# Kernel tuning notes

Measured on AMD Instinct MI355X. Metric: run time of the kernel, lower is better.

Reference implementation:

```python
import jax, jax.numpy as jnp
import numpy as np
from jax import lax

# db6 filters (pywt convention). rec_lo are the standard Daubechies-12 scaling coefs.
REC_LO = np.array([0.11154074335008017, 0.4946238903983854, 0.7511339080215775,
                   0.3152503517092432, -0.22626469396516913, -0.12976686756709563,
                   0.09750160558707936, 0.02752286553001629, -0.031582039318031156,
                   0.0005538422009938016, 0.004777257511010651, -0.00107730108499558])
L = 12
# qmf: rec_hi[n] = (-1)^n * rec_lo[L-1-n]
REC_HI = np.array([(-1.0)**n * REC_LO[L - 1 - n] for n in range(L)])
DEC_LO = REC_LO[::-1].copy()
DEC_HI = REC_HI[::-1].copy()
J = 8  # level1
DN = ('NCH', 'OIH', 'NCH')

def _afb(x):
    # one analysis level, symmetric padding (matches pytorch_wavelets afb1d).
    B, C, N = x.shape
    outsize = (N + L - 1) // 2
    p = 2 * (outsize - 1) - N + L
    xp = jnp.pad(x, ((0, 0), (0, 0), (p // 2, p - p // 2)), mode='symmetric')
    # torch conv1d correlates with reversed dec filters == rec filters
    k = jnp.stack([jnp.asarray(REC_LO, x.dtype), jnp.asarray(REC_HI, x.dtype)])[:, None, :]
    y = lax.conv_general_dilated(xp.reshape(B * C, 1, -1), k, (2,), 'VALID',
                                 dimension_numbers=DN)  # (B*C, 2, outsize)
    y = y.reshape(B, C, 2, outsize)
    return y[:, :, 0], y[:, :, 1]

def _sfb(lo, hi):
    # one synthesis level: conv_transpose1d(stride=2, padding=L-2) with rec filters
    # == dilate-by-2, pad 1 each side, correlate with flipped rec (= dec) filters.
    B, C, N = lo.shape
    def up(z, k):
        kk = jnp.asarray(k, z.dtype)[None, None, :]
        return lax.conv_general_dilated(z.reshape(B * C, 1, N), kk, (1,), [(1, 1)],
                                        lhs_dilation=(2,), dimension_numbers=DN).reshape(B, C, -1)
    return up(lo, DEC_LO) + up(hi, DEC_HI)  # length 2N - L + 2

def setup_inputs() -> dict:
    key = jax.random.key(0)
    k1, k2, k3 = jax.random.split(key, 3)
    Cin, Cout = 64, 64
    scale = 1.0 / (Cin * Cout)
    x = jax.random.normal(k1, (256, Cin, 1024), dtype=jnp.float32)
    weights1 = scale * jax.random.uniform(k2, (Cin, Cout, J + 6), dtype=jnp.float32)
    weights2 = scale * jax.random.uniform(k3, (Cin, Cout, J + 6), dtype=jnp.float32)
    return {'x': x, 'weights1': weights1, 'weights2': weights2}

def reference(x, weights1, weights2):
    # DWT decompose: yh[0] finest ... yh[-1] coarsest (pytorch_wavelets order)
    lo = x
    highs = []
    for _ in range(J):
        lo, hi = _afb(lo)
        highs.append(hi)
    # channel mix on coarsest approx and coarsest detail
    lo = jnp.einsum('bix,iox->box', lo, weights1)
    highs[-1] = jnp.einsum('bix,iox->box', highs[-1], weights2)
    # IDWT reconstruct, trimming odd-length mismatches like pytorch_wavelets
    y = lo
    for hi in highs[::-1]:
        if y.shape[-1] > hi.shape[-1]:
            y = y[..., :hi.shape[-1]]
        y = _sfb(y, hi)
    return y
```

## Files before the change

### kernel.cpp

```cpp
#include <hip/hip_runtime.h>

typedef float f2 __attribute__((ext_vector_type(2)));
typedef _Float16 half_t;
typedef _Float16 h4 __attribute__((ext_vector_type(4)));
typedef _Float16 h8 __attribute__((ext_vector_type(8)));

static constexpr float REC_LO[12] = {
  0.11154074335008017f, 0.4946238903983854f, 0.7511339080215775f, 0.3152503517092432f,
  -0.22626469396516913f, -0.12976686756709563f, 0.09750160558707936f, 0.02752286553001629f,
  -0.031582039318031156f, 0.0005538422009938016f, 0.004777257511010651f, -0.00107730108499558f };
static constexpr float REC_HI[12] = {
  -0.00107730108499558f, -0.004777257511010651f, 0.0005538422009938016f, 0.031582039318031156f,
  0.02752286553001629f, -0.09750160558707936f, -0.12976686756709563f, 0.22626469396516913f,
  0.3152503517092432f, -0.7511339080215775f, 0.4946238903983854f, -0.11154074335008017f };
static constexpr float DEC_LO[12] = {
  -0.00107730108499558f, 0.004777257511010651f, 0.0005538422009938016f, -0.031582039318031156f,
  0.02752286553001629f, 0.09750160558707936f, -0.12976686756709563f, -0.22626469396516913f,
  0.3152503517092432f, 0.7511339080215775f, 0.4946238903983854f, 0.11154074335008017f };
static constexpr float DEC_HI[12] = {
  -0.11154074335008017f, 0.4946238903983854f, -0.7511339080215775f, 0.3152503517092432f,
  0.22626469396516913f, -0.12976686756709563f, -0.09750160558707936f, 0.02752286553001629f,
  0.031582039318031156f, 0.0005538422009938016f, -0.004777257511010651f, -0.00107730108499558f };

#define NROWS 16384
#define WPB 4


__global__ __launch_bounds__(256) void afb_fused(const float* __restrict__ x,
                                                 half_t* __restrict__ ws) {
  __shared__ float sA[WPB][548];
  __shared__ float sB[WPB][296];
  constexpr int LENS[9] = {1024, 517, 264, 137, 74, 42, 26, 18, 14};
  constexpr int HSTR[8] = {520, 264, 144, 80, 48, 32, 24, 16};
  constexpr int HOFF[8] = {0, 520, 784, 928, 1008, 1056, 1088, 1112};
  const int wid = threadIdx.x >> 6;
  const int lane = threadIdx.x & 63;
  const int row = blockIdx.x * WPB + wid;
  float* bufA = sA[wid];
  float* bufB = sB[wid];
  const float* xrow = x + (size_t)row * 1024;
  half_t* hi0 = ws + (size_t)row * 520;

  {
    const int q = lane;
    const int base = (q == 0) ? 0 : 16 * q - 12;
    float xv[28];
#pragma unroll
    for (int r = 0; r < 7; ++r) {
      float4 v = *reinterpret_cast<const float4*>(xrow + base + 4 * r);
      xv[4 * r] = v.x; xv[4 * r + 1] = v.y; xv[4 * r + 2] = v.z; xv[4 * r + 3] = v.w;
    }
    float w[26];
    if (q == 0) {
#pragma unroll
      for (int e = 0; e < 26; ++e) w[e] = xv[e < 10 ? 9 - e : e - 10];
    } else {
#pragma unroll
      for (int e = 0; e < 26; ++e) w[e] = xv[2 + e];
    }
    f2 a[8];
#pragma unroll
    for (int d = 0; d < 8; ++d) a[d] = (f2){0.f, 0.f};
#pragma unroll
    for (int k = 0; k < 12; ++k) {
      f2 c = (f2){REC_LO[k], REC_HI[k]};
#pragma unroll
      for (int d = 0; d < 8; ++d) a[d] += w[2 * d + k] * c;
    }
#pragma unroll
    for (int d = 0; d < 4; ++d)
      *reinterpret_cast<f2*>(bufA + 14 + 8 * q + 2 * d) = (f2){a[2 * d].x, a[2 * d + 1].x};
    h8 hh;
#pragma unroll
    for (int d = 0; d < 8; ++d) hh[d] = (half_t)a[d].y;
    *reinterpret_cast<h8*>(hi0 + 8 * q) = hh;
  }
  if (lane < 5) {
    const int i0 = 1014 + 2 * lane;
    float acL = 0.f, acH = 0.f;
#pragma unroll
    for (int k = 0; k < 12; ++k) {
      int idx = i0 + k;
      idx = min(idx, 2047 - idx);
      float v = xrow[idx];
      acL += v * REC_LO[k];
      acH += v * REC_HI[k];
    }
    bufA[14 + 512 + lane] = acL;
    hi0[512 + lane] = (half_t)acH;
  }
  if (lane < 21) {
    int d, s;
    if (lane < 10) { d = 13 - lane; s = 14 + lane; }
    else { int k = lane - 10; d = 14 + 517 + k; s = 14 + 516 - k; }
    bufA[d] = bufA[s];
  }

  if (lane < 33) {
    const float* pp = bufA + 16 * lane + 4;
    float xv[28];
#pragma unroll
    for (int r = 0; r < 7; ++r) {
      float4 v = *reinterpret_cast<const float4*>(pp + 4 * r);
      xv[4 * r] = v.x; xv[4 * r + 1] = v.y; xv[4 * r + 2] = v.z; xv[4 * r + 3] = v.w;
    }
    f2 a[8];
#pragma unroll
    for (int d = 0; d < 8; ++d) a[d] = (f2){0.f, 0.f};
#pragma unroll
    for (int k = 0; k < 12; ++k) {
      f2 c = (f2){REC_LO[k], REC_HI[k]};
#pragma unroll
      for (int d = 0; d < 8; ++d) a[d] += xv[2 * d + k] * c;
    }
#pragma unroll
    for (int d = 0; d < 4; ++d)
      *reinterpret_cast<f2*>(bufB + 14 + 8 * lane + 2 * d) = (f2){a[2 * d].x, a[2 * d + 1].x};
    h8 hh;
#pragma unroll
    for (int d = 0; d < 8; ++d) hh[d] = (half_t)a[d].y;
    *reinterpret_cast<h8*>(ws + (size_t)NROWS * 520 + (size_t)row * 264 + 8 * lane) = hh;
  }
  if (lane < 21) {
    int d, s;
    if (lane < 10) { d = 13 - lane; s = 14 + lane; }
    else { int k = lane - 10; d = 14 + 264 + k; s = 14 + 263 - k; }
    bufB[d] = bufB[s];
  }

  float* cur = bufB;
  float* dst = bufA;
#pragma unroll
  for (int j = 2; j < 8; ++j) {
    const int outN = LENS[j + 1];
    const int NCH = (outN + 3) / 4;
    half_t* hiRow = ws + (size_t)NROWS * HOFF[j] + (size_t)row * HSTR[j];
    if (lane < NCH) {
      const float* pp = cur + 8 * lane + 4;
      float xv[20];
#pragma unroll
      for (int r = 0; r < 5; ++r) {
        float4 v = *reinterpret_cast<const float4*>(pp + 4 * r);
        xv[4 * r] = v.x; xv[4 * r + 1] = v.y; xv[4 * r + 2] = v.z; xv[4 * r + 3] = v.w;
      }
      f2 a0 = {0.f, 0.f}, a1 = {0.f, 0.f}, a2 = {0.f, 0.f}, a3 = {0.f, 0.f};
#pragma unroll
      for (int k = 0; k < 12; ++k) {
        f2 c = (f2){REC_LO[k], REC_HI[k]};
        a0 += xv[k] * c; a1 += xv[2 + k] * c; a2 += xv[4 + k] * c; a3 += xv[6 + k] * c;
      }
      if (j < 7) {
        *reinterpret_cast<f2*>(dst + 14 + 4 * lane) = (f2){a0.x, a1.x};
        *reinterpret_cast<f2*>(dst + 16 + 4 * lane) = (f2){a2.x, a3.x};
      } else {
        h4 hl; hl[0] = (half_t)a0.x; hl[1] = (half_t)a1.x; hl[2] = (half_t)a2.x; hl[3] = (half_t)a3.x;
        *reinterpret_cast<h4*>(ws + (size_t)NROWS * 1128 + (size_t)row * 16 + 4 * lane) = hl;
      }
      h4 hh; hh[0] = (half_t)a0.y; hh[1] = (half_t)a1.y; hh[2] = (half_t)a2.y; hh[3] = (half_t)a3.y;
      *reinterpret_cast<h4*>(hiRow + 4 * lane) = hh;
    }
    if (j < 7) {
      if (lane < 21) {
        int d, s;
        if (lane < 10) { d = 13 - lane; s = 14 + lane; }
        else { int k = lane - 10; d = 14 + outN + k; s = 14 + outN - 1 - k; }
        dst[d] = dst[s];
      }
      float* t = cur; cur = dst; dst = t;
    }
  }
}

__global__ __launch_bounds__(256) void sfb_fused(const half_t* __restrict__ ws,
                                                 float* __restrict__ out) {
  __shared__ float sP[WPB][280];
  __shared__ float sQ[WPB][544];
  constexpr int LENSY[8] = {14, 18, 26, 42, 74, 137, 264, 517};
  constexpr int HSOFF[8] = {1144, 1088, 1056, 1008, 928, 784, 520, 0};
  constexpr int HSSTR[8] = {16, 24, 32, 48, 80, 144, 264, 520};
  const int wid = threadIdx.x >> 6;
  const int lane = threadIdx.x & 63;
  const int row = blockIdx.x * WPB + wid;
  float* ping = sP[wid];
  float* pong = sQ[wid];

  if (lane < 2) {
    h8 v = *reinterpret_cast<const h8*>(ws + (size_t)NROWS * 1160 + (size_t)row * 16 + 8 * lane);
    *reinterpret_cast<float4*>(ping + 8 * lane) =
        make_float4((float)v[0], (float)v[1], (float)v[2], (float)v[3]);
    *reinterpret_cast<float4*>(ping + 8 * lane + 4) =
        make_float4((float)v[4], (float)v[5], (float)v[6], (float)v[7]);
  }

  float* cur = ping;
  float* dst = pong;
#pragma unroll
  for (int s = 0; s < 8; ++s) {
    const int N = LENSY[s];
    const int NP = N - 5;
    const int PCH = (NP + 3) / 4;
    const half_t* hsrc = ws + (size_t)NROWS * HSOFF[s] + (size_t)row * HSSTR[s];
#pragma unroll
    for (int q0 = 0; q0 < PCH; q0 += 64) {
      int q = q0 + lane;
      if (q < PCH) {
        const int m0 = 4 * q;
        float lv[9];
        {
          float4 a = *reinterpret_cast<const float4*>(cur + m0);
          float4 b = *reinterpret_cast<const float4*>(cur + m0 + 4);
          lv[0] = a.x; lv[1] = a.y; lv[2] = a.z; lv[3] = a.w;
          lv[4] = b.x; lv[5] = b.y; lv[6] = b.z; lv[7] = b.w;
          lv[8] = cur[m0 + 8];
        }
        float hv[9];
        {
          h4 h0 = *reinterpret_cast<const h4*>(hsrc + m0);
          h4 h1 = *reinterpret_cast<const h4*>(hsrc + m0 + 4);
          half_t h2 = hsrc[m0 + 8];
          hv[0] = (float)h0[0]; hv[1] = (float)h0[1]; hv[2] = (float)h0[2]; hv[3] = (float)h0[3];
          hv[4] = (float)h1[0]; hv[5] = (float)h1[1]; hv[6] = (float)h1[2]; hv[7] = (float)h1[3];
          hv[8] = (float)h2;
        }
        f2 a0 = {0.f, 0.f}, a1 = {0.f, 0.f}, a2 = {0.f, 0.f}, a3 = {0.f, 0.f};
#pragma unroll
        for (int t = 0; t < 6; ++t) {
          f2 dl = (f2){DEC_LO[2 * t + 1], DEC_LO[2 * t]};
          f2 dh = (f2){DEC_HI[2 * t + 1], DEC_HI[2 * t]};
          a0 += lv[t] * dl + hv[t] * dh;
          a1 += lv[1 + t] * dl + hv[1 + t] * dh;
          a2 += lv[2 + t] * dl + hv[2 + t] * dh;
          a3 += lv[3 + t] * dl + hv[3 + t] * dh;
        }
        if (s < 7) {
          *reinterpret_cast<float4*>(dst + 2 * m0)     = make_float4(a0.x, a0.y, a1.x, a1.y);
          *reinterpret_cast<float4*>(dst + 2 * m0 + 4) = make_float4(a2.x, a2.y, a3.x, a3.y);
        } else {
          float* orow = out + (size_t)row * 1024 + 2 * m0;
          *reinterpret_cast<float4*>(orow)     = make_float4(a0.x, a0.y, a1.x, a1.y);
          *reinterpret_cast<float4*>(orow + 4) = make_float4(a2.x, a2.y, a3.x, a3.y);
        }
      }
    }
    if (s < 7) { float* t = cur; cur = dst; dst = t; }
  }
}

__global__ void mix_both(half_t* __restrict__ ws, const float* __restrict__ w1,
                         const float* __restrict__ w2) {
  __shared__ float s_in[4][896];
  const int which = blockIdx.x >> 6;
  const half_t* in = ws + (size_t)NROWS * (which ? 1112 : 1128);
  const float* w = which ? w2 : w1;
  half_t* out = ws + (size_t)NROWS * (which ? 1144 : 1160);
  int b0 = (blockIdx.x & 63) * 4;
  int t = threadIdx.x;
  int i = t / 14, xx = t % 14;
#pragma unroll
  for (int bb = 0; bb < 4; ++bb)
    s_in[bb][t] = (float)in[((size_t)(b0 + bb) * 64 + i) * 16 + xx];
  __syncthreads();
  float acc[4] = {0.f, 0.f, 0.f, 0.f};
#pragma unroll 8
  for (int k = 0; k < 64; ++k) {
    float wv = w[k * 896 + t];
#pragma unroll
    for (int bb = 0; bb < 4; ++bb) acc[bb] += s_in[bb][k * 14 + xx] * wv;
  }
#pragma unroll
  for (int bb = 0; bb < 4; ++bb)
    out[((size_t)(b0 + bb) * 64 + i) * 16 + xx] = (half_t)acc[bb];
}

extern "C" void kernel_launch(void* const* d_in, const int* in_sizes, int n_in,
                              void* d_out, int out_size, void* d_ws, size_t ws_size,
                              hipStream_t stream) {
  (void)in_sizes; (void)n_in; (void)out_size; (void)ws_size;
  const float* x  = (const float*)d_in[0];
  const float* w1 = (const float*)d_in[1];
  const float* w2 = (const float*)d_in[2];
  float* out = (float*)d_out;
  half_t* ws = (half_t*)d_ws;

  afb_fused<<<NROWS / WPB, 64 * WPB, 0, stream>>>(x, ws);
  mix_both<<<128, 896, 0, stream>>>(ws, w1, w2);
  sfb_fused<<<NROWS / WPB, 64 * WPB, 0, stream>>>(ws, out);
}
```

Before: 71.56 us.

## Pack four rows into one wavefront for short DWT levels, split mix blocks

```diff
diff --git a/kernel.cpp b/kernel.cpp
--- a/kernel.cpp
+++ b/kernel.cpp
@@ -128,44 +128,50 @@
     bufB[d] = bufB[s];
   }
 
-  float* cur = bufB;
-  float* dst = bufA;
+  __syncthreads();
+  if (wid != 0) return;
+
+  const int sub = lane >> 4, l16 = lane & 15;
+  const int prow = blockIdx.x * WPB + sub;
+  float* cur = sB[sub];
+  float* dst = sA[sub];
+  constexpr int NITS[8] = {0, 0, 3, 2, 1, 1, 1, 1};
 #pragma unroll
   for (int j = 2; j < 8; ++j) {
     const int outN = LENS[j + 1];
     const int NCH = (outN + 3) / 4;
-    half_t* hiRow = ws + (size_t)NROWS * HOFF[j] + (size_t)row * HSTR[j];
-    if (lane < NCH) {
-      const float* pp = cur + 8 * lane + 4;
-      float xv[20];
-#pragma unroll
-      for (int r = 0; r < 5; ++r) {
-        float4 v = *reinterpret_cast<const float4*>(pp + 4 * r);
-        xv[4 * r] = v.x; xv[4 * r + 1] = v.y; xv[4 * r + 2] = v.z; xv[4 * r + 3] = v.w;
-      }
-      f2 a0 = {0.f, 0.f}, a1 = {0.f, 0.f}, a2 = {0.f, 0.f}, a3 = {0.f, 0.f};
-#pragma unroll
-      for (int k = 0; k < 12; ++k) {
-        f2 c = (f2){REC_LO[k], REC_HI[k]};
-        a0 += xv[k] * c; a1 += xv[2 + k] * c; a2 += xv[4 + k] * c; a3 += xv[6 + k] * c;
-      }
-      if (j < 7) {
-        *reinterpret_cast<f2*>(dst + 14 + 4 * lane) = (f2){a0.x, a1.x};
-        *reinterpret_cast<f2*>(dst + 16 + 4 * lane) = (f2){a2.x, a3.x};
-      } else {
-        h4 hl; hl[0] = (half_t)a0.x; hl[1] = (half_t)a1.x; hl[2] = (half_t)a2.x; hl[3] = (half_t)a3.x;
-        *reinterpret_cast<h4*>(ws + (size_t)NROWS * 1128 + (size_t)row * 16 + 4 * lane) = hl;
-      }
-      h4 hh; hh[0] = (half_t)a0.y; hh[1] = (half_t)a1.y; hh[2] = (half_t)a2.y; hh[3] = (half_t)a3.y;
-      *reinterpret_cast<h4*>(hiRow + 4 * lane) = hh;
+    half_t* hiRow = ws + (size_t)NROWS * HOFF[j] + (size_t)prow * HSTR[j];
+#pragma unroll
+    for (int it = 0; it < NITS[j]; ++it) {
+      const int q = it * 16 + l16;
+      if (q < NCH) {
+        const float* pp = cur + 8 * q + 4;
+        float xv[20];
+#pragma unroll
+        for (int r = 0; r < 5; ++r) {
+          float4 v = *reinterpret_cast<const float4*>(pp + 4 * r);
+          xv[4 * r] = v.x; xv[4 * r + 1] = v.y; xv[4 * r + 2] = v.z; xv[4 * r + 3] = v.w;
+        }
+        f2 a0 = {0.f, 0.f}, a1 = {0.f, 0.f}, a2 = {0.f, 0.f}, a3 = {0.f, 0.f};
+#pragma unroll
+        for (int k = 0; k < 12; ++k) {
+          f2 c = (f2){REC_LO[k], REC_HI[k]};
+          a0 += xv[k] * c; a1 += xv[2 + k] * c; a2 += xv[4 + k] * c; a3 += xv[6 + k] * c;
+        }
+        if (j < 7) {
+          *reinterpret_cast<f2*>(dst + 14 + 4 * q) = (f2){a0.x, a1.x};
+          *reinterpret_cast<f2*>(dst + 16 + 4 * q) = (f2){a2.x, a3.x};
+        } else {
+          h4 hl; hl[0] = (half_t)a0.x; hl[1] = (half_t)a1.x; hl[2] = (half_t)a2.x; hl[3] = (half_t)a3.x;
+          *reinterpret_cast<h4*>(ws + (size_t)NROWS * 1128 + (size_t)prow * 16 + 4 * q) = hl;
+        }
+        h4 hh; hh[0] = (half_t)a0.y; hh[1] = (half_t)a1.y; hh[2] = (half_t)a2.y; hh[3] = (half_t)a3.y;
+        *reinterpret_cast<h4*>(hiRow + 4 * q) = hh;
+      }
     }
     if (j < 7) {
-      if (lane < 21) {
-        int d, s;
-        if (lane < 10) { d = 13 - lane; s = 14 + lane; }
-        else { int k = lane - 10; d = 14 + outN + k; s = 14 + outN - 1 - k; }
-        dst[d] = dst[s];
-      }
+      if (l16 < 10) dst[13 - l16] = dst[14 + l16];
+      if (l16 < 11) dst[14 + outN + l16] = dst[14 + outN - 1 - l16];
       float* t = cur; cur = dst; dst = t;
     }
   }
@@ -175,35 +181,81 @@
                                                  float* __restrict__ out) {
   __shared__ float sP[WPB][280];
   __shared__ float sQ[WPB][544];
-  constexpr int LENSY[8] = {14, 18, 26, 42, 74, 137, 264, 517};
-  constexpr int HSOFF[8] = {1144, 1088, 1056, 1008, 928, 784, 520, 0};
-  constexpr int HSSTR[8] = {16, 24, 32, 48, 80, 144, 264, 520};
   const int wid = threadIdx.x >> 6;
   const int lane = threadIdx.x & 63;
+
+  if (wid == 0) {
+    constexpr int LENSY[6] = {14, 18, 26, 42, 74, 137};
+    constexpr int HSOFF[6] = {1144, 1088, 1056, 1008, 928, 784};
+    constexpr int HSSTR[6] = {16, 24, 32, 48, 80, 144};
+    constexpr int NITS[6] = {1, 1, 1, 1, 2, 3};
+    const int sub = lane >> 4, l16 = lane & 15;
+    const int prow = blockIdx.x * WPB + sub;
+    float* cur = sP[sub];
+    float* dst = sQ[sub];
+    if (l16 < 2) {
+      h8 v = *reinterpret_cast<const h8*>(ws + (size_t)NROWS * 1160 + (size_t)prow * 16 + 8 * l16);
+      *reinterpret_cast<float4*>(cur + 8 * l16) =
+          make_float4((float)v[0], (float)v[1], (float)v[2], (float)v[3]);
+      *reinterpret_cast<float4*>(cur + 8 * l16 + 4) =
+          make_float4((float)v[4], (float)v[5], (float)v[6], (float)v[7]);
+    }
+#pragma unroll
+    for (int s = 0; s < 6; ++s) {
+      const int N = LENSY[s];
+      const int NP = N - 5;
+      const int PCH = (NP + 3) / 4;
+      const half_t* hsrc = ws + (size_t)NROWS * HSOFF[s] + (size_t)prow * HSSTR[s];
+#pragma unroll
+      for (int it = 0; it < NITS[s]; ++it) {
+        const int q = it * 16 + l16;
+        if (q < PCH) {
+          const int m0 = 4 * q;
+          float lv[9];
+          {
+            float4 a = *reinterpret_cast<const float4*>(cur + m0);
+            float4 b = *reinterpret_cast<const float4*>(cur + m0 + 4);
+            lv[0] = a.x; lv[1] = a.y; lv[2] = a.z; lv[3] = a.w;
+            lv[4] = b.x; lv[5] = b.y; lv[6] = b.z; lv[7] = b.w;
+            lv[8] = cur[m0 + 8];
+          }
+          float hv[9];
+          {
+            h4 h0 = *reinterpret_cast<const h4*>(hsrc + m0);
+            h4 h1 = *reinterpret_cast<const h4*>(hsrc + m0 + 4);
+            half_t h2 = hsrc[m0 + 8];
+            hv[0] = (float)h0[0]; hv[1] = (float)h0[1]; hv[2] = (float)h0[2]; hv[3] = (float)h0[3];
+            hv[4] = (float)h1[0]; hv[5] = (float)h1[1]; hv[6] = (float)h1[2]; hv[7] = (float)h1[3];
+            hv[8] = (float)h2;
+          }
+          f2 a0 = {0.f, 0.f}, a1 = {0.f, 0.f}, a2 = {0.f, 0.f}, a3 = {0.f, 0.f};
+#pragma unroll
+          for (int t = 0; t < 6; ++t) {
+            f2 dl = (f2){DEC_LO[2 * t + 1], DEC_LO[2 * t]};
+            f2 dh = (f2){DEC_HI[2 * t + 1], DEC_HI[2 * t]};
+            a0 += lv[t] * dl + hv[t] * dh;
+            a1 += lv[1 + t] * dl + hv[1 + t] * dh;
+            a2 += lv[2 + t] * dl + hv[2 + t] * dh;
+            a3 += lv[3 + t] * dl + hv[3 + t] * dh;
+          }
+          *reinterpret_cast<float4*>(dst + 2 * m0)     = make_float4(a0.x, a0.y, a1.x, a1.y);
+          *reinterpret_cast<float4*>(dst + 2 * m0 + 4) = make_float4(a2.x, a2.y, a3.x, a3.y);
+        }
+      }
+      float* t = cur; cur = dst; dst = t;
+    }
+  }
+  __syncthreads();
+
   const int row = blockIdx.x * WPB + wid;
-  float* ping = sP[wid];
-  float* pong = sQ[wid];
-
-  if (lane < 2) {
-    h8 v = *reinterpret_cast<const h8*>(ws + (size_t)NROWS * 1160 + (size_t)row * 16 + 8 * lane);
-    *reinterpret_cast<float4*>(ping + 8 * lane) =
-        make_float4((float)v[0], (float)v[1], (float)v[2], (float)v[3]);
-    *reinterpret_cast<float4*>(ping + 8 * lane + 4) =
-        make_float4((float)v[4], (float)v[5], (float)v[6], (float)v[7]);
-  }
-
-  float* cur = ping;
-  float* dst = pong;
-#pragma unroll
-  for (int s = 0; s < 8; ++s) {
-    const int N = LENSY[s];
-    const int NP = N - 5;
-    const int PCH = (NP + 3) / 4;
-    const half_t* hsrc = ws + (size_t)NROWS * HSOFF[s] + (size_t)row * HSSTR[s];
-#pragma unroll
-    for (int q0 = 0; q0 < PCH; q0 += 64) {
-      int q = q0 + lane;
-      if (q < PCH) {
+  float* cur = sP[wid];
+  float* dst = sQ[wid];
+  {
+    const half_t* hsrc = ws + (size_t)NROWS * 520 + (size_t)row * 264;
+#pragma unroll
+    for (int q0 = 0; q0 < 65; q0 += 64) {
+      const int q = q0 + lane;
+      if (q < 65) {
         const int m0 = 4 * q;
         float lv[9];
         {
@@ -232,44 +284,73 @@
           a2 += lv[2 + t] * dl + hv[2 + t] * dh;
           a3 += lv[3 + t] * dl + hv[3 + t] * dh;
         }
-        if (s < 7) {
-          *reinterpret_cast<float4*>(dst + 2 * m0)     = make_float4(a0.x, a0.y, a1.x, a1.y);
-          *reinterpret_cast<float4*>(dst + 2 * m0 + 4) = make_float4(a2.x, a2.y, a3.x, a3.y);
-        } else {
-          float* orow = out + (size_t)row * 1024 + 2 * m0;
-          *reinterpret_cast<float4*>(orow)     = make_float4(a0.x, a0.y, a1.x, a1.y);
-          *reinterpret_cast<float4*>(orow + 4) = make_float4(a2.x, a2.y, a3.x, a3.y);
-        }
-      }
-    }
-    if (s < 7) { float* t = cur; cur = dst; dst = t; }
+        *reinterpret_cast<float4*>(dst + 2 * m0)     = make_float4(a0.x, a0.y, a1.x, a1.y);
+        *reinterpret_cast<float4*>(dst + 2 * m0 + 4) = make_float4(a2.x, a2.y, a3.x, a3.y);
+      }
+    }
+  }
+  {
+    const half_t* hsrc = ws + (size_t)row * 520;
+    float* orow = out + (size_t)row * 1024;
+#pragma unroll
+    for (int q0 = 0; q0 < 128; q0 += 64) {
+      const int m0 = 4 * (q0 + lane);
+      float lv[9];
+      {
+        float4 a = *reinterpret_cast<const float4*>(dst + m0);
+        float4 b = *reinterpret_cast<const float4*>(dst + m0 + 4);
+        lv[0] = a.x; lv[1] = a.y; lv[2] = a.z; lv[3] = a.w;
+        lv[4] = b.x; lv[5] = b.y; lv[6] = b.z; lv[7] = b.w;
+        lv[8] = dst[m0 + 8];
+      }
+      float hv[9];
+      {
+        h4 h0 = *reinterpret_cast<const h4*>(hsrc + m0);
+        h4 h1 = *reinterpret_cast<const h4*>(hsrc + m0 + 4);
+        half_t h2 = hsrc[m0 + 8];
+        hv[0] = (float)h0[0]; hv[1] = (float)h0[1]; hv[2] = (float)h0[2]; hv[3] = (float)h0[3];
+        hv[4] = (float)h1[0]; hv[5] = (float)h1[1]; hv[6] = (float)h1[2]; hv[7] = (float)h1[3];
+        hv[8] = (float)h2;
+      }
+      f2 a0 = {0.f, 0.f}, a1 = {0.f, 0.f}, a2 = {0.f, 0.f}, a3 = {0.f, 0.f};
+#pragma unroll
+      for (int t = 0; t < 6; ++t) {
+        f2 dl = (f2){DEC_LO[2 * t + 1], DEC_LO[2 * t]};
+        f2 dh = (f2){DEC_HI[2 * t + 1], DEC_HI[2 * t]};
+        a0 += lv[t] * dl + hv[t] * dh;
+        a1 += lv[1 + t] * dl + hv[1 + t] * dh;
+        a2 += lv[2 + t] * dl + hv[2 + t] * dh;
+        a3 += lv[3 + t] * dl + hv[3 + t] * dh;
+      }
+      *reinterpret_cast<float4*>(orow + 2 * m0)     = make_float4(a0.x, a0.y, a1.x, a1.y);
+      *reinterpret_cast<float4*>(orow + 2 * m0 + 4) = make_float4(a2.x, a2.y, a3.x, a3.y);
+    }
   }
 }
 
 __global__ void mix_both(half_t* __restrict__ ws, const float* __restrict__ w1,
                          const float* __restrict__ w2) {
-  __shared__ float s_in[4][896];
-  const int which = blockIdx.x >> 6;
+  __shared__ float s_in[2][896];
+  const int which = blockIdx.x >> 7;
   const half_t* in = ws + (size_t)NROWS * (which ? 1112 : 1128);
   const float* w = which ? w2 : w1;
   half_t* out = ws + (size_t)NROWS * (which ? 1144 : 1160);
-  int b0 = (blockIdx.x & 63) * 4;
+  int b0 = (blockIdx.x & 127) * 2;
   int t = threadIdx.x;
   int i = t / 14, xx = t % 14;
 #pragma unroll
-  for (int bb = 0; bb < 4; ++bb)
+  for (int bb = 0; bb < 2; ++bb)
     s_in[bb][t] = (float)in[((size_t)(b0 + bb) * 64 + i) * 16 + xx];
   __syncthreads();
-  float acc[4] = {0.f, 0.f, 0.f, 0.f};
+  float acc0 = 0.f, acc1 = 0.f;
 #pragma unroll 8
   for (int k = 0; k < 64; ++k) {
     float wv = w[k * 896 + t];
-#pragma unroll
-    for (int bb = 0; bb < 4; ++bb) acc[bb] += s_in[bb][k * 14 + xx] * wv;
-  }
-#pragma unroll
-  for (int bb = 0; bb < 4; ++bb)
-    out[((size_t)(b0 + bb) * 64 + i) * 16 + xx] = (half_t)acc[bb];
+    acc0 += s_in[0][k * 14 + xx] * wv;
+    acc1 += s_in[1][k * 14 + xx] * wv;
+  }
+  out[((size_t)b0 * 64 + i) * 16 + xx] = (half_t)acc0;
+  out[((size_t)(b0 + 1) * 64 + i) * 16 + xx] = (half_t)acc1;
 }
 
 extern "C" void kernel_launch(void* const* d_in, const int* in_sizes, int n_in,
@@ -283,6 +364,6 @@
   half_t* ws = (half_t*)d_ws;
 
   afb_fused<<<NROWS / WPB, 64 * WPB, 0, stream>>>(x, ws);
-  mix_both<<<128, 896, 0, stream>>>(ws, w1, w2);
+  mix_both<<<256, 896, 0, stream>>>(ws, w1, w2);
   sfb_fused<<<NROWS / WPB, 64 * WPB, 0, stream>>>(ws, out);
 }
```

Measured after the change: 63.28 us. 1.13x faster.
